# Kernel optimization log

Hardware: AMD Instinct MI355X
Metric: run time of the kernel (lower is better)

## Reference

```python
import jax, jax.numpy as jnp
import numpy as np

EPS = 1e-5

def _ln(x):
    # LayerNorm over last dim, no affine (elementwise_affine=False), biased variance
    mu = jnp.mean(x, axis=-1, keepdims=True)
    var = jnp.mean(jnp.square(x - mu), axis=-1, keepdims=True)
    return (x - mu) / jnp.sqrt(var + EPS)

def setup_inputs() -> dict:
    key = jax.random.key(0)
    B, I, H = 32768, 512, 512
    ks = jax.random.split(key, 12)
    std = 1.0 / np.sqrt(H)
    u = lambda k, shape: jax.random.uniform(k, shape, jnp.float32, -std, std)
    return {
        "x": jax.random.normal(ks[0], (B, I), jnp.float32),
        "h": jax.random.normal(ks[1], (B, H), jnp.float32),
        "W_i2h": u(ks[2], (I, 2 * H)),
        "b_i2h": u(ks[3], (2 * H,)),
        "W_h2h": u(ks[4], (H, 2 * H)),
        "b_h2h": u(ks[5], (2 * H,)),
        "W_hatW": u(ks[6], (I, H)),
        "b_hatW": u(ks[7], (H,)),
        "W_hatU": u(ks[8], (H, H)),
        "b_hatU": u(ks[9], (H,)),
    }

def reference(x, h, W_i2h, b_i2h, W_h2h, b_h2h, W_hatW, b_hatW, W_hatU, b_hatU):
    H = W_hatU.shape[0]
    i2h = _ln(x @ W_i2h + b_i2h)          # [B, 2H]
    h2h = _ln(h @ W_h2h + b_h2h)          # [B, 2H]
    gates = jax.nn.sigmoid(i2h + h2h)
    z_t = gates[:, :H]
    r_t = gates[:, -H:]
    h_hat_first = _ln(x @ W_hatW + b_hatW)  # [B, H]
    h_hat_last = _ln(h @ W_hatU + b_hatU)   # [B, H]
    h_hat = jnp.tanh(h_hat_first + r_t * h_hat_last)
    h_t = (1.0 - z_t) * h + z_t * h_hat
    return h_t
```

## Files before the change

### kernel.cpp

```cpp
#include <hip/hip_runtime.h>
#include <stdint.h>

typedef unsigned short u16;
typedef __attribute__((ext_vector_type(8))) short short8;
typedef __attribute__((ext_vector_type(4))) short short4v;
typedef __attribute__((ext_vector_type(4))) float f4;
typedef __attribute__((ext_vector_type(4))) float f32x4;

static __device__ __forceinline__ u16 f2b(float f) {
  union { float f; uint32_t u; } c; c.f = f;
  return (u16)((c.u + 0x7FFFu + ((c.u >> 16) & 1u)) >> 16);
}
static __device__ __forceinline__ float b2f(u16 s) {
  union { uint32_t u; float f; } c; c.u = ((uint32_t)s) << 16; return c.f;
}

__global__ __launch_bounds__(256) void cvt_kernel(const float* __restrict__ x,
                                                  const float* __restrict__ h,
                                                  u16* __restrict__ Ab) {
  const size_t half = (size_t)32768 * 512;
  size_t tid = (size_t)blockIdx.x * blockDim.x + threadIdx.x;
  size_t nth = (size_t)gridDim.x * blockDim.x;
  size_t total8 = (half * 2) >> 3;
  for (size_t t = tid; t < total8; t += nth) {
    size_t e = t << 3;
    const float* src = (e < half) ? (x + e) : (h + (e - half));
    f4 v0 = *(const f4*)src;
    f4 v1 = *(const f4*)(src + 4);
    short8 o;
    o[0] = (short)f2b(v0[0]); o[1] = (short)f2b(v0[1]);
    o[2] = (short)f2b(v0[2]); o[3] = (short)f2b(v0[3]);
    o[4] = (short)f2b(v1[0]); o[5] = (short)f2b(v1[1]);
    o[6] = (short)f2b(v1[2]); o[7] = (short)f2b(v1[3]);
    *(short8*)(Ab + e) = o;
  }
}

__global__ __launch_bounds__(256) void transpose_cat(const float* __restrict__ srcA,
                                                     const float* __restrict__ srcB,
                                                     u16* __restrict__ dst,
                                                     int NA, int NB) {
  __shared__ float t[32][33];
  int n0 = blockIdx.x * 32, k0 = blockIdx.y * 32;
  int tx = threadIdx.x, ty = threadIdx.y;
  const float* src; int strideN, nb;
  if (n0 < NA) { src = srcA; strideN = NA; nb = n0; }
  else         { src = srcB; strideN = NB; nb = n0 - NA; }
#pragma unroll
  for (int i = 0; i < 4; ++i) {
    int k = k0 + ty + i * 8;
    t[tx][ty + i * 8] = src[(size_t)k * strideN + nb + tx];
  }
  __syncthreads();
#pragma unroll
  for (int i = 0; i < 4; ++i) {
    int n = ty + i * 8;
    dst[(size_t)(n0 + n) * 512 + k0 + tx] = f2b(t[n][tx]);
  }
}

#define AS1 __attribute__((address_space(1)))
#define AS3 __attribute__((address_space(3)))

__global__ __launch_bounds__(512, 2) void gemm_kernel(
    const u16* __restrict__ Ab, const u16* __restrict__ WxT,
    const u16* __restrict__ WhT, u16* __restrict__ Cb,
    int rowStartX, int rowStartH, int tilesPerHalf) {
  __shared__ u16 lds[65536];

  int tid = threadIdx.x, lane = tid & 63, wv = tid >> 6;
  int wm = wv >> 2, wn = wv & 3;
  int l15 = lane & 15, l4 = lane >> 4;

  int nwg = gridDim.x, bid = blockIdx.x;
  int swz = (nwg & 7) ? bid : ((bid & 7) * (nwg >> 3) + (bid >> 3));
  int mb = swz / 6, nb = swz - mb * 6;
  size_t m0; const u16* Wt;
  if (mb < tilesPerHalf) { m0 = (size_t)rowStartX + (size_t)mb * 256; Wt = WxT; }
  else { m0 = (size_t)rowStartH + (size_t)(mb - tilesPerHalf) * 256; Wt = WhT; }
  int crow0 = mb * 256, n0 = nb * 256;

  int idx0 = wv * 128 + lane, idx1 = idx0 + 64;
  int r0 = idx0 >> 2, c0 = (idx0 & 3) ^ ((r0 ^ (r0 >> 2)) & 3);
  int r1 = idx1 >> 2, c1 = (idx1 & 3) ^ ((r1 ^ (r1 >> 2)) & 3);
  const u16* sA0 = Ab + (m0 + r0) * 512 + c0 * 8;
  const u16* sA1 = Ab + (m0 + r1) * 512 + c1 * 8;
  const u16* sB0 = Wt + (size_t)(n0 + r0) * 512 + c0 * 8;
  const u16* sB1 = Wt + (size_t)(n0 + r1) * 512 + c1 * 8;
  int dOffA = wv * 1024;

  int gl = (l15 ^ (l15 >> 2)) & 3;
  int slot = l4 ^ gl;
  int aOff = (wm * 128 + l15) * 32 + slot * 8;
  int bOff = 8192 + (wn * 64 + l15) * 32 + slot * 8;

  f32x4 acc[8][4] = {};

#define STG(t) do { \
    u16* _b = lds + (((t) & 3) << 14); \
    __builtin_amdgcn_global_load_lds((const AS1 void*)(sA0 + (t) * 32), (AS3 void*)(_b + dOffA), 16, 0, 0); \
    __builtin_amdgcn_global_load_lds((const AS1 void*)(sA1 + (t) * 32), (AS3 void*)(_b + dOffA + 512), 16, 0, 0); \
    __builtin_amdgcn_global_load_lds((const AS1 void*)(sB0 + (t) * 32), (AS3 void*)(_b + 8192 + dOffA), 16, 0, 0); \
    __builtin_amdgcn_global_load_lds((const AS1 void*)(sB1 + (t) * 32), (AS3 void*)(_b + 8192 + dOffA + 512), 16, 0, 0); \
  } while (0)

  STG(0); STG(1); STG(2);
  asm volatile("s_waitcnt vmcnt(8)" ::: "memory");
  __builtin_amdgcn_sched_barrier(0);
  __builtin_amdgcn_s_barrier();
  __builtin_amdgcn_sched_barrier(0);

#pragma unroll
  for (int t = 0; t < 16; ++t) {
    const u16* buf = lds + ((t & 3) << 14);
    if (t < 13) STG(t + 3);
    short8 bfr[4], afr[8];
#pragma unroll
    for (int nr = 0; nr < 4; ++nr) bfr[nr] = *(const short8*)(buf + bOff + nr * 512);
#pragma unroll
    for (int mr = 0; mr < 8; ++mr) afr[mr] = *(const short8*)(buf + aOff + mr * 512);
    __builtin_amdgcn_s_setprio(1);
#pragma unroll
    for (int mr = 0; mr < 8; ++mr)
#pragma unroll
      for (int nr = 0; nr < 4; ++nr)
        acc[mr][nr] = __builtin_amdgcn_mfma_f32_16x16x32_bf16(
            bfr[nr], afr[mr], acc[mr][nr], 0, 0, 0);
    __builtin_amdgcn_s_setprio(0);
    if (t < 13)       { asm volatile("s_waitcnt vmcnt(8)" ::: "memory"); }
    else if (t == 13) { asm volatile("s_waitcnt vmcnt(4)" ::: "memory"); }
    else if (t == 14) { asm volatile("s_waitcnt vmcnt(0)" ::: "memory"); }
    if (t < 15) {
      __builtin_amdgcn_sched_barrier(0);
      __builtin_amdgcn_s_barrier();
      __builtin_amdgcn_sched_barrier(0);
    }
  }
#undef STG

#pragma unroll
  for (int mr = 0; mr < 8; ++mr) {
    int m = crow0 + wm * 128 + mr * 16 + l15;
#pragma unroll
    for (int nr = 0; nr < 4; ++nr) {
      int n = n0 + wn * 64 + nr * 16 + l4 * 4;
      short4v o;
      o[0] = (short)f2b(acc[mr][nr][0]);
      o[1] = (short)f2b(acc[mr][nr][1]);
      o[2] = (short)f2b(acc[mr][nr][2]);
      o[3] = (short)f2b(acc[mr][nr][3]);
      *(short4v*)(Cb + (size_t)m * 1536 + n) = o;
    }
  }
}

__global__ __launch_bounds__(256) void epi_kernel(
    const u16* __restrict__ Cb, const float* __restrict__ h,
    const float* __restrict__ b_i2h, const float* __restrict__ b_h2h,
    const float* __restrict__ b_hatW, const float* __restrict__ b_hatU,
    float* __restrict__ out, int mBase, int BC) {
  int wv = threadIdx.x >> 6;
  int lane = threadIdx.x & 63;
  int mLocal = blockIdx.x * 4 + wv;
  size_t mGlob = (size_t)mBase + mLocal;
  const u16* Ar = Cb + (size_t)mLocal * 1536;
  const u16* Br = Cb + ((size_t)BC + mLocal) * 1536;
  int j0 = lane * 8;

  float a[3][8], b[3][8];
#pragma unroll
  for (int c = 0; c < 3; ++c) {
    short8 va = *(const short8*)(Ar + c * 512 + j0);
    short8 vb = *(const short8*)(Br + c * 512 + j0);
    const float* biasA = (c == 0) ? (b_i2h + j0) : (c == 1) ? (b_i2h + 512 + j0) : (b_hatW + j0);
    const float* biasB = (c == 0) ? (b_h2h + j0) : (c == 1) ? (b_h2h + 512 + j0) : (b_hatU + j0);
    f4 ba0 = *(const f4*)biasA, ba1 = *(const f4*)(biasA + 4);
    f4 bb0 = *(const f4*)biasB, bb1 = *(const f4*)(biasB + 4);
#pragma unroll
    for (int j = 0; j < 4; ++j) {
      a[c][j]     = b2f((u16)va[j])     + ba0[j];
      a[c][j + 4] = b2f((u16)va[j + 4]) + ba1[j];
      b[c][j]     = b2f((u16)vb[j])     + bb0[j];
      b[c][j + 4] = b2f((u16)vb[j + 4]) + bb1[j];
    }
  }

  float s1a = 0, q1a = 0, s2a = 0, q2a = 0, s1b = 0, q1b = 0, s2b = 0, q2b = 0;
#pragma unroll
  for (int j = 0; j < 8; ++j) {
    s1a += a[0][j] + a[1][j]; q1a += a[0][j] * a[0][j] + a[1][j] * a[1][j];
    s2a += a[2][j];           q2a += a[2][j] * a[2][j];
    s1b += b[0][j] + b[1][j]; q1b += b[0][j] * b[0][j] + b[1][j] * b[1][j];
    s2b += b[2][j];           q2b += b[2][j] * b[2][j];
  }
#pragma unroll
  for (int off = 32; off > 0; off >>= 1) {
    s1a += __shfl_xor(s1a, off); q1a += __shfl_xor(q1a, off);
    s2a += __shfl_xor(s2a, off); q2a += __shfl_xor(q2a, off);
    s1b += __shfl_xor(s1b, off); q1b += __shfl_xor(q1b, off);
    s2b += __shfl_xor(s2b, off); q2b += __shfl_xor(q2b, off);
  }
  const float inv1 = 1.0f / 1024.0f, inv2 = 1.0f / 512.0f, eps = 1e-5f;
  float mu1a = s1a * inv1, mu2a = s2a * inv2, mu1b = s1b * inv1, mu2b = s2b * inv2;
  float rs1a = rsqrtf(q1a * inv1 - mu1a * mu1a + eps);
  float rs2a = rsqrtf(q2a * inv2 - mu2a * mu2a + eps);
  float rs1b = rsqrtf(q1b * inv1 - mu1b * mu1b + eps);
  float rs2b = rsqrtf(q2b * inv2 - mu2b * mu2b + eps);

  const float* hrow = h + mGlob * 512 + j0;
  f4 h0 = *(const f4*)hrow, h1 = *(const f4*)(hrow + 4);
  f4 o0, o1;
#pragma unroll
  for (int j = 0; j < 8; ++j) {
    float zs  = (a[0][j] - mu1a) * rs1a + (b[0][j] - mu1b) * rs1b;
    float rsg = (a[1][j] - mu1a) * rs1a + (b[1][j] - mu1b) * rs1b;
    float z = 1.0f / (1.0f + __expf(-zs));
    float r = 1.0f / (1.0f + __expf(-rsg));
    float hh = tanhf((a[2][j] - mu2a) * rs2a + r * ((b[2][j] - mu2b) * rs2b));
    float hv = (j < 4) ? h0[j] : h1[j - 4];
    float o = hv + z * (hh - hv);
    if (j < 4) o0[j] = o; else o1[j - 4] = o;
  }
  *(f4*)(out + mGlob * 512 + j0) = o0;
  *(f4*)(out + mGlob * 512 + j0 + 4) = o1;
}

extern "C" void kernel_launch(void* const* d_in, const int* in_sizes, int n_in,
                              void* d_out, int out_size, void* d_ws, size_t ws_size,
                              hipStream_t stream) {
  const float* x      = (const float*)d_in[0];
  const float* h      = (const float*)d_in[1];
  const float* W_i2h  = (const float*)d_in[2];
  const float* b_i2h  = (const float*)d_in[3];
  const float* W_h2h  = (const float*)d_in[4];
  const float* b_h2h  = (const float*)d_in[5];
  const float* W_hatW = (const float*)d_in[6];
  const float* b_hatW = (const float*)d_in[7];
  const float* W_hatU = (const float*)d_in[8];
  const float* b_hatU = (const float*)d_in[9];
  float* out = (float*)d_out;

  u16* WxT = (u16*)d_ws;
  u16* WhT = WxT + (size_t)1536 * 512;
  u16* Ab  = WhT + (size_t)1536 * 512;
  u16* Cb  = Ab + (size_t)65536 * 512;

  size_t fixedElems = (size_t)2 * 1536 * 512 + (size_t)65536 * 512;
  int chunks = 1;
  for (;;) {
    size_t need = (fixedElems + (size_t)2 * (32768 / chunks) * 1536) * sizeof(u16);
    if (need <= ws_size || chunks >= 128) break;
    chunks <<= 1;
  }
  int BC = 32768 / chunks;
  int tph = BC / 256;
  int nwg = 2 * tph * 6;

  cvt_kernel<<<2048, 256, 0, stream>>>(x, h, Ab);
  transpose_cat<<<dim3(48, 16), dim3(32, 8), 0, stream>>>(W_i2h, W_hatW, WxT, 1024, 512);
  transpose_cat<<<dim3(48, 16), dim3(32, 8), 0, stream>>>(W_h2h, W_hatU, WhT, 1024, 512);
  for (int cc = 0; cc < chunks; ++cc) {
    gemm_kernel<<<nwg, 512, 0, stream>>>(Ab, WxT, WhT, Cb,
                                         cc * BC, 32768 + cc * BC, tph);
    epi_kernel<<<BC / 4, 256, 0, stream>>>(Cb, h, b_i2h, b_h2h, b_hatW, b_hatU,
                                           out, cc * BC, BC);
  }
}
```

Before: 251.0 us.

## Restructure GEMM mainloop to 64-wide K tiles with double-buffered LDS and phased MFMA

The bf16 GEMM mainloop now uses a 64-element K step, cutting the loop to 8 iterations, with two LDS buffers instead of four 32-wide ones. The global-to-LDS copy layout and XOR swizzle are rewritten for 128-byte rows. Each iteration is split into four barrier-separated phases that interleave LDS fragment loads with MFMA groups, ping-pong style. The aim is fewer loop iterations and better overlap of LDS reads with matrix math. In exchange, prefetch depth drops to one tile, each iteration waits on vmcnt(0), and there are more workgroup barriers per iteration.

```diff
diff --git a/kernel.cpp b/kernel.cpp
--- a/kernel.cpp
+++ b/kernel.cpp
@@ -61,6 +61,7 @@
 
 #define AS1 __attribute__((address_space(1)))
 #define AS3 __attribute__((address_space(3)))
+#define SBAR0 __builtin_amdgcn_sched_barrier(0)
 
 __global__ __launch_bounds__(512, 2) void gemm_kernel(
     const u16* __restrict__ Ab, const u16* __restrict__ WxT,
@@ -80,61 +81,93 @@
   else { m0 = (size_t)rowStartH + (size_t)(mb - tilesPerHalf) * 256; Wt = WhT; }
   int crow0 = mb * 256, n0 = nb * 256;
 
-  int idx0 = wv * 128 + lane, idx1 = idx0 + 64;
-  int r0 = idx0 >> 2, c0 = (idx0 & 3) ^ ((r0 ^ (r0 >> 2)) & 3);
-  int r1 = idx1 >> 2, c1 = (idx1 & 3) ^ ((r1 ^ (r1 >> 2)) & 3);
-  const u16* sA0 = Ab + (m0 + r0) * 512 + c0 * 8;
-  const u16* sA1 = Ab + (m0 + r1) * 512 + c1 * 8;
-  const u16* sB0 = Wt + (size_t)(n0 + r0) * 512 + c0 * 8;
-  const u16* sB1 = Wt + (size_t)(n0 + r1) * 512 + c1 * 8;
-  int dOffA = wv * 1024;
-
-  int gl = (l15 ^ (l15 >> 2)) & 3;
-  int slot = l4 ^ gl;
-  int aOff = (wm * 128 + l15) * 32 + slot * 8;
-  int bOff = 8192 + (wn * 64 + l15) * 32 + slot * 8;
+  int rr = wv * 8 + (lane >> 3);
+  int g8 = ((lane & 7) ^ (lane >> 3)) * 8;
+  const u16* pA[4]; const u16* pB[4];
+#pragma unroll
+  for (int i = 0; i < 4; ++i) {
+    pA[i] = Ab + (m0 + i * 64 + rr) * 512 + g8;
+    pB[i] = Wt + (size_t)(n0 + i * 64 + rr) * 512 + g8;
+  }
+  int dst = wv * 512;
+
+#define STG(t) do { \
+    int _bb = ((t) & 1) << 15; \
+    int _ko = (t) << 6; \
+    _Pragma("unroll") \
+    for (int i = 0; i < 4; ++i) { \
+      __builtin_amdgcn_global_load_lds((const AS1 void*)(pA[i] + _ko), \
+          (AS3 void*)(lds + _bb + i * 4096 + dst), 16, 0, 0); \
+      __builtin_amdgcn_global_load_lds((const AS1 void*)(pB[i] + _ko), \
+          (AS3 void*)(lds + _bb + 16384 + i * 4096 + dst), 16, 0, 0); \
+    } \
+  } while (0)
+
+  int sl0 = (l4 ^ (l15 & 7)) * 8;
+  int sl1 = ((4 + l4) ^ (l15 & 7)) * 8;
+  int aRow = (wm * 128 + l15) * 64;
+  int bRow = 16384 + (wn * 64 + l15) * 64;
 
   f32x4 acc[8][4] = {};
 
-#define STG(t) do { \
-    u16* _b = lds + (((t) & 3) << 14); \
-    __builtin_amdgcn_global_load_lds((const AS1 void*)(sA0 + (t) * 32), (AS3 void*)(_b + dOffA), 16, 0, 0); \
-    __builtin_amdgcn_global_load_lds((const AS1 void*)(sA1 + (t) * 32), (AS3 void*)(_b + dOffA + 512), 16, 0, 0); \
-    __builtin_amdgcn_global_load_lds((const AS1 void*)(sB0 + (t) * 32), (AS3 void*)(_b + 8192 + dOffA), 16, 0, 0); \
-    __builtin_amdgcn_global_load_lds((const AS1 void*)(sB1 + (t) * 32), (AS3 void*)(_b + 8192 + dOffA + 512), 16, 0, 0); \
-  } while (0)
-
-  STG(0); STG(1); STG(2);
+  STG(0); STG(1);
   asm volatile("s_waitcnt vmcnt(8)" ::: "memory");
-  __builtin_amdgcn_sched_barrier(0);
-  __builtin_amdgcn_s_barrier();
-  __builtin_amdgcn_sched_barrier(0);
-
-#pragma unroll
-  for (int t = 0; t < 16; ++t) {
-    const u16* buf = lds + ((t & 3) << 14);
-    if (t < 13) STG(t + 3);
-    short8 bfr[4], afr[8];
-#pragma unroll
-    for (int nr = 0; nr < 4; ++nr) bfr[nr] = *(const short8*)(buf + bOff + nr * 512);
-#pragma unroll
-    for (int mr = 0; mr < 8; ++mr) afr[mr] = *(const short8*)(buf + aOff + mr * 512);
+  SBAR0; __builtin_amdgcn_s_barrier(); SBAR0;
+
+  for (int t = 0; t < 8; ++t) {
+    const u16* buf = lds + ((t & 1) << 15);
+    short8 afr[4], bfr[4];
+    if (t >= 1 && t < 7) STG(t + 1);
+#pragma unroll
+    for (int nr = 0; nr < 4; ++nr) bfr[nr] = *(const short8*)(buf + bRow + nr * 1024 + sl0);
+#pragma unroll
+    for (int mr = 0; mr < 4; ++mr) afr[mr] = *(const short8*)(buf + aRow + mr * 1024 + sl0);
+    SBAR0; __builtin_amdgcn_s_barrier(); SBAR0;
     __builtin_amdgcn_s_setprio(1);
 #pragma unroll
-    for (int mr = 0; mr < 8; ++mr)
+    for (int mr = 0; mr < 4; ++mr)
 #pragma unroll
       for (int nr = 0; nr < 4; ++nr)
-        acc[mr][nr] = __builtin_amdgcn_mfma_f32_16x16x32_bf16(
-            bfr[nr], afr[mr], acc[mr][nr], 0, 0, 0);
+        acc[mr][nr] = __builtin_amdgcn_mfma_f32_16x16x32_bf16(bfr[nr], afr[mr], acc[mr][nr], 0, 0, 0);
     __builtin_amdgcn_s_setprio(0);
-    if (t < 13)       { asm volatile("s_waitcnt vmcnt(8)" ::: "memory"); }
-    else if (t == 13) { asm volatile("s_waitcnt vmcnt(4)" ::: "memory"); }
-    else if (t == 14) { asm volatile("s_waitcnt vmcnt(0)" ::: "memory"); }
-    if (t < 15) {
-      __builtin_amdgcn_sched_barrier(0);
+#pragma unroll
+    for (int mr = 0; mr < 4; ++mr) afr[mr] = *(const short8*)(buf + aRow + (mr + 4) * 1024 + sl0);
+    SBAR0; __builtin_amdgcn_s_barrier(); SBAR0;
+    __builtin_amdgcn_s_setprio(1);
+#pragma unroll
+    for (int mr = 0; mr < 4; ++mr)
+#pragma unroll
+      for (int nr = 0; nr < 4; ++nr)
+        acc[mr + 4][nr] = __builtin_amdgcn_mfma_f32_16x16x32_bf16(bfr[nr], afr[mr], acc[mr + 4][nr], 0, 0, 0);
+    __builtin_amdgcn_s_setprio(0);
+#pragma unroll
+    for (int nr = 0; nr < 4; ++nr) bfr[nr] = *(const short8*)(buf + bRow + nr * 1024 + sl1);
+#pragma unroll
+    for (int mr = 0; mr < 4; ++mr) afr[mr] = *(const short8*)(buf + aRow + mr * 1024 + sl1);
+    SBAR0; __builtin_amdgcn_s_barrier(); SBAR0;
+    __builtin_amdgcn_s_setprio(1);
+#pragma unroll
+    for (int mr = 0; mr < 4; ++mr)
+#pragma unroll
+      for (int nr = 0; nr < 4; ++nr)
+        acc[mr][nr] = __builtin_amdgcn_mfma_f32_16x16x32_bf16(bfr[nr], afr[mr], acc[mr][nr], 0, 0, 0);
+    __builtin_amdgcn_s_setprio(0);
+#pragma unroll
+    for (int mr = 0; mr < 4; ++mr) afr[mr] = *(const short8*)(buf + aRow + (mr + 4) * 1024 + sl1);
+    SBAR0; __builtin_amdgcn_s_barrier(); SBAR0;
+    __builtin_amdgcn_s_setprio(1);
+#pragma unroll
+    for (int mr = 0; mr < 4; ++mr)
+#pragma unroll
+      for (int nr = 0; nr < 4; ++nr)
+        acc[mr + 4][nr] = __builtin_amdgcn_mfma_f32_16x16x32_bf16(bfr[nr], afr[mr], acc[mr + 4][nr], 0, 0, 0);
+    __builtin_amdgcn_s_setprio(0);
+    SBAR0;
+    if (t < 7) {
+      asm volatile("s_waitcnt vmcnt(0)" ::: "memory");
       __builtin_amdgcn_s_barrier();
-      __builtin_amdgcn_sched_barrier(0);
     }
+    SBAR0;
   }
 #undef STG
 
```

Result: no change. 246.5 us (-1.8%).
